# Optimization experiments

Hardware: AMD Instinct MI355X
Metric: run time of the kernel (lower is better)

## Reference

```python
import jax, jax.numpy as jnp
import numpy as np

NOISE = 0.001
SHAPE = (8, 15, 512, 512)  # (n_b, n_t, n_x, n_y)
OBS_FRACTION = 0.3         # fraction of entries that are valid observations


def setup_inputs() -> dict:
    key = jax.random.key(0)
    kx, ki, km = jax.random.split(key, 3)
    x = jax.random.normal(kx, SHAPE, dtype=jnp.float32)
    inp = jax.random.normal(ki, SHAPE, dtype=jnp.float32)
    # Simulate sparse observations: non-observed entries are NaN (isfinite mask).
    obs_mask = jax.random.uniform(km, SHAPE) < OBS_FRACTION
    inp = jnp.where(obs_mask, inp, jnp.float32(jnp.nan))
    return {"x": x, "inp": inp}


def reference(x, inp):
    # Original: per-batch sparse H selects finite entries of flatten(x[i]),
    # m = obs - H x, NLobs[i] = -(m^T (1/noise I) m) = -(1/noise) * sum(m^2).
    mask = jnp.isfinite(inp)
    diff = jnp.where(mask, inp - x, jnp.float32(0.0))
    # Reduce over (t, x, y) -> per-batch scalar, shape [n_b]
    return (-1.0 / NOISE) * jnp.sum(diff * diff, axis=(1, 2, 3))
```

## Files before the change

### kernel.cpp

```cpp
#include <hip/hip_runtime.h>
#include <math.h>


constexpr int N_B = 8;
constexpr long long N_PER_BATCH = 15LL * 512 * 512;
constexpr int BLOCKS_PER_BATCH = 256;
constexpr int THREADS = 256;
constexpr float NEG_INV_NOISE = -1000.0f;

__device__ __forceinline__ float wave_reduce_add(float v) {
    #pragma unroll
    for (int off = 32; off > 0; off >>= 1)
        v += __shfl_down(v, off, 64);
    return v;
}

__global__ __launch_bounds__(THREADS)
void nlpobs_partial(const float* __restrict__ x,
                    const float* __restrict__ inp,
                    float* __restrict__ partial) {
    const int b   = blockIdx.x / BLOCKS_PER_BATCH;
    const int blk = blockIdx.x % BLOCKS_PER_BATCH;

    const float4* __restrict__ x4 = reinterpret_cast<const float4*>(x   + (size_t)b * N_PER_BATCH);
    const float4* __restrict__ i4 = reinterpret_cast<const float4*>(inp + (size_t)b * N_PER_BATCH);
    const int n4 = (int)(N_PER_BATCH / 4);

    float acc = 0.0f;
    for (int i = blk * THREADS + threadIdx.x; i < n4; i += BLOCKS_PER_BATCH * THREADS) {
        float4 xv = x4[i];
        float4 iv = i4[i];
        float d0 = iv.x - xv.x;
        float d1 = iv.y - xv.y;
        float d2 = iv.z - xv.z;
        float d3 = iv.w - xv.w;
        acc += isfinite(iv.x) ? d0 * d0 : 0.0f;
        acc += isfinite(iv.y) ? d1 * d1 : 0.0f;
        acc += isfinite(iv.z) ? d2 * d2 : 0.0f;
        acc += isfinite(iv.w) ? d3 * d3 : 0.0f;
    }

    acc = wave_reduce_add(acc);
    __shared__ float lds[THREADS / 64];
    const int lane = threadIdx.x & 63;
    const int wave = threadIdx.x >> 6;
    if (lane == 0) lds[wave] = acc;
    __syncthreads();
    if (threadIdx.x == 0) {
        float s = 0.0f;
        #pragma unroll
        for (int w = 0; w < THREADS / 64; ++w) s += lds[w];
        partial[blockIdx.x] = s;
    }
}

__global__ __launch_bounds__(THREADS)
void nlpobs_final(const float* __restrict__ partial,
                  float* __restrict__ out) {
    const int b = blockIdx.x;
    float acc = partial[b * BLOCKS_PER_BATCH + threadIdx.x];
    acc = wave_reduce_add(acc);
    __shared__ float lds[THREADS / 64];
    const int lane = threadIdx.x & 63;
    const int wave = threadIdx.x >> 6;
    if (lane == 0) lds[wave] = acc;
    __syncthreads();
    if (threadIdx.x == 0) {
        float s = 0.0f;
        #pragma unroll
        for (int w = 0; w < THREADS / 64; ++w) s += lds[w];
        out[b] = NEG_INV_NOISE * s;
    }
}

extern "C" void kernel_launch(void* const* d_in, const int* in_sizes, int n_in,
                              void* d_out, int out_size, void* d_ws, size_t ws_size,
                              hipStream_t stream) {
    const float* x   = (const float*)d_in[0];
    const float* inp = (const float*)d_in[1];
    float* out       = (float*)d_out;
    float* partial   = (float*)d_ws;

    nlpobs_partial<<<N_B * BLOCKS_PER_BATCH, THREADS, 0, stream>>>(x, inp, partial);
    nlpobs_final<<<N_B, THREADS, 0, stream>>>(partial, out);
}
```

Before: 43.83 us.

## Fuse final reduction via last-block atomic counter and unroll fixed-trip loop

Replaces the two-kernel reduction with a single kernel in which the last block of each batch, detected with an atomic counter and threadfence, sums the partial results. The main loop becomes a fixed trip count (15) with unroll 3 so more loads are in flight. The goal is to drop the second kernel launch and its gap, and to improve memory-level parallelism. A hipMemsetAsync is now needed to reset the counters, which adds its own operation to each call.

```diff
diff --git a/kernel.cpp b/kernel.cpp
--- a/kernel.cpp
+++ b/kernel.cpp
@@ -6,6 +6,8 @@
 constexpr long long N_PER_BATCH = 15LL * 512 * 512;
 constexpr int BLOCKS_PER_BATCH = 256;
 constexpr int THREADS = 256;
+constexpr int STRIDE = BLOCKS_PER_BATCH * THREADS;
+constexpr int TRIPS = (int)(N_PER_BATCH / 4 / STRIDE);
 constexpr float NEG_INV_NOISE = -1000.0f;
 
 __device__ __forceinline__ float wave_reduce_add(float v) {
@@ -15,19 +17,37 @@
     return v;
 }
 
+__device__ __forceinline__ float block_reduce_add(float v, float* lds) {
+    v = wave_reduce_add(v);
+    const int lane = threadIdx.x & 63;
+    const int wave = threadIdx.x >> 6;
+    if (lane == 0) lds[wave] = v;
+    __syncthreads();
+    float s = 0.0f;
+    if (threadIdx.x == 0) {
+        #pragma unroll
+        for (int w = 0; w < THREADS / 64; ++w) s += lds[w];
+    }
+    return s;
+}
+
 __global__ __launch_bounds__(THREADS)
-void nlpobs_partial(const float* __restrict__ x,
-                    const float* __restrict__ inp,
-                    float* __restrict__ partial) {
+void nlpobs_fused(const float* __restrict__ x,
+                  const float* __restrict__ inp,
+                  float* __restrict__ partial,
+                  unsigned int* __restrict__ counters,
+                  float* __restrict__ out) {
     const int b   = blockIdx.x / BLOCKS_PER_BATCH;
     const int blk = blockIdx.x % BLOCKS_PER_BATCH;
 
     const float4* __restrict__ x4 = reinterpret_cast<const float4*>(x   + (size_t)b * N_PER_BATCH);
     const float4* __restrict__ i4 = reinterpret_cast<const float4*>(inp + (size_t)b * N_PER_BATCH);
-    const int n4 = (int)(N_PER_BATCH / 4);
 
     float acc = 0.0f;
-    for (int i = blk * THREADS + threadIdx.x; i < n4; i += BLOCKS_PER_BATCH * THREADS) {
+    const int base = blk * THREADS + threadIdx.x;
+    #pragma unroll 3
+    for (int k = 0; k < TRIPS; ++k) {
+        const int i = base + k * STRIDE;
         float4 xv = x4[i];
         float4 iv = i4[i];
         float d0 = iv.x - xv.x;
@@ -40,37 +60,24 @@
         acc += isfinite(iv.w) ? d3 * d3 : 0.0f;
     }
 
-    acc = wave_reduce_add(acc);
     __shared__ float lds[THREADS / 64];
-    const int lane = threadIdx.x & 63;
-    const int wave = threadIdx.x >> 6;
-    if (lane == 0) lds[wave] = acc;
+    __shared__ bool is_last;
+    float s = block_reduce_add(acc, lds);
+
+    if (threadIdx.x == 0) {
+        partial[blockIdx.x] = s;
+        __threadfence();
+        unsigned int prev = atomicAdd(&counters[b], 1u);
+        is_last = (prev == BLOCKS_PER_BATCH - 1);
+    }
     __syncthreads();
-    if (threadIdx.x == 0) {
-        float s = 0.0f;
-        #pragma unroll
-        for (int w = 0; w < THREADS / 64; ++w) s += lds[w];
-        partial[blockIdx.x] = s;
-    }
-}
+    if (!is_last) return;
 
-__global__ __launch_bounds__(THREADS)
-void nlpobs_final(const float* __restrict__ partial,
-                  float* __restrict__ out) {
-    const int b = blockIdx.x;
-    float acc = partial[b * BLOCKS_PER_BATCH + threadIdx.x];
-    acc = wave_reduce_add(acc);
-    __shared__ float lds[THREADS / 64];
-    const int lane = threadIdx.x & 63;
-    const int wave = threadIdx.x >> 6;
-    if (lane == 0) lds[wave] = acc;
+    __threadfence();
+    float v = partial[b * BLOCKS_PER_BATCH + threadIdx.x];
     __syncthreads();
-    if (threadIdx.x == 0) {
-        float s = 0.0f;
-        #pragma unroll
-        for (int w = 0; w < THREADS / 64; ++w) s += lds[w];
-        out[b] = NEG_INV_NOISE * s;
-    }
+    float total = block_reduce_add(v, lds);
+    if (threadIdx.x == 0) out[b] = NEG_INV_NOISE * total;
 }
 
 extern "C" void kernel_launch(void* const* d_in, const int* in_sizes, int n_in,
@@ -79,8 +86,10 @@
     const float* x   = (const float*)d_in[0];
     const float* inp = (const float*)d_in[1];
     float* out       = (float*)d_out;
-    float* partial   = (float*)d_ws;
 
-    nlpobs_partial<<<N_B * BLOCKS_PER_BATCH, THREADS, 0, stream>>>(x, inp, partial);
-    nlpobs_final<<<N_B, THREADS, 0, stream>>>(partial, out);
+    float* partial         = (float*)d_ws;
+    unsigned int* counters = (unsigned int*)((char*)d_ws + 2048 * sizeof(float));
+
+    hipMemsetAsync(counters, 0, N_B * sizeof(unsigned int), stream);
+    nlpobs_fused<<<N_B * BLOCKS_PER_BATCH, THREADS, 0, stream>>>(x, inp, partial, counters, out);
 }
```

Measured after the change: 115.6 us. +163.8%, slower.
